# Kernel tuning notes

Hardware: AMD Instinct MI355X
Metric: run time of the kernel (lower is better)

## Reference

```python
import jax, jax.numpy as jnp
import numpy as np

WSZ = 16   # cfg.window_size
GD = 64    # cfg.group_dim


def setup_inputs() -> dict:
    key = jax.random.key(0)
    k1, k2, k3, k4 = jax.random.split(key, 4)
    B, T, D = 8, 8192, 1024
    z = jax.random.normal(k1, (B, T, D), jnp.float32)
    token_lens = jax.random.randint(k2, (B, T), 1, 9).astype(jnp.int32)
    W1 = jax.random.normal(k3, (D, GD), jnp.float32) / np.sqrt(D)
    W2 = jax.random.normal(k4, (GD, GD), jnp.float32) / np.sqrt(GD)
    return {"z": z, "token_lens": token_lens, "W1": W1, "W2": W2, "target_len": 6144}


def _choose_pairs(local_sim, budget):
    # local_sim: (W-1,) sims of adjacent edges inside one window.
    # Greedy non-overlapping matching in descending-sim order, up to `budget` pairs.
    Wn = local_sim.shape[0] + 1
    order = jnp.argsort(-local_sim)

    def step(state, e):
        used, mr, picked = state
        ok = (picked < budget) & (~used[e]) & (~used[e + 1])
        used = used.at[e].set(used[e] | ok)
        used = used.at[e + 1].set(used[e + 1] | ok)
        mr = mr.at[e + 1].set(mr[e + 1] | ok)
        return (used, mr, picked + ok.astype(jnp.int32)), None

    init = (jnp.zeros(Wn, bool), jnp.zeros(Wn, bool), jnp.int32(0))
    (_, mr, _), _ = jax.lax.scan(step, init, order)
    return mr  # (W,) True at j -> merge token j into j-1


def reference(z, token_lens, W1, W2, target_len):
    B, T, D = z.shape
    nwin = T // WSZ  # T chosen divisible by WSZ -> all windows full
    merges_needed = T - target_len
    base, extra = merges_needed // nwin, merges_needed % nwin
    budgets = jnp.minimum(base + (jnp.arange(nwin) < extra), WSZ // 2).astype(jnp.int32)

    # grouping MLP + cosine-style adjacent similarity
    g = jnp.maximum(z @ W1, 0.0) @ W2                         # (B,T,GD)
    g = g / (jnp.linalg.norm(g, axis=-1, keepdims=True) + 1e-8)
    sim = jnp.sum(g[:, :-1] * g[:, 1:], axis=-1)              # (B,T-1)
    # pad boundary edge slot, view per-window; keep only intra-window edges
    sim_pad = jnp.pad(sim, ((0, 0), (0, 1)), constant_values=-jnp.inf)
    local = sim_pad.reshape(B, nwin, WSZ)[:, :, : WSZ - 1]    # (B,nwin,W-1)

    pick = jax.vmap(jax.vmap(_choose_pairs, in_axes=(0, 0)), in_axes=(0, None))
    merge_right = pick(local, budgets).reshape(B, T)          # (B,T) bool
    keep = ~merge_right

    # pairs are disjoint -> sequential torch loop == parallel weighted merge
    w = token_lens.astype(z.dtype)
    absorb = merge_right[:, 1:]                               # token i absorbs i+1
    wi, wj = w[:, :-1, None], w[:, 1:, None]
    merged = (z[:, :-1] * wi + z[:, 1:] * wj) / (wi + wj)
    z2 = jnp.concatenate([jnp.where(absorb[:, :, None], merged, z[:, :-1]), z[:, -1:]], axis=1)
    l2 = jnp.concatenate(
        [jnp.where(absorb, token_lens[:, :-1] + token_lens[:, 1:], token_lens[:, :-1]),
         token_lens[:, -1:]], axis=1)

    # stable compaction: kept indices first (order preserved), truncate
    order = jnp.argsort(~keep, axis=1)[:, :target_len]        # jax sort is stable
    z_new = jnp.take_along_axis(z2, order[:, :, None], axis=1)
    lens_new = jnp.take_along_axis(l2, order, axis=1)
    starts_new = jnp.cumsum(lens_new, axis=1) - lens_new
    return z_new, lens_new, starts_new
```

## Files before the change

kernel.cpp:

```cpp
#include <hip/hip_runtime.h>

#define B_ 8
#define T_ 8192
#define D_ 1024
#define GD_ 64
#define WSZ_ 16
#define NWIN_ (T_ / WSZ_)
#define PL1_ (4 * 32 * 512)
#define PL2_ (4 * 2 * 512)

typedef __attribute__((ext_vector_type(8))) short short8v;
typedef __attribute__((ext_vector_type(4))) float f32x4;

__device__ __forceinline__ unsigned bf16rne(unsigned u) {
  return (u + 0x7FFFu + ((u >> 16) & 1u)) >> 16;
}
__device__ __forceinline__ void split2(float x, short& h, short& m) {
  const unsigned uh = bf16rne(__float_as_uint(x));
  const float fh = __uint_as_float(uh << 16);
  const float r1 = x - fh;
  const unsigned um = bf16rne(__float_as_uint(r1));
  h = (short)uh; m = (short)um;
}

__global__ __launch_bounds__(256) void k_prep(
    const float* __restrict__ W1, const float* __restrict__ W2,
    short* __restrict__ w1f, short* __restrict__ w2f)
{
  const int i = blockIdx.x * 256 + threadIdx.x;
  if (i < 4 * 32 * 64 * 8) {
    const int e = i & 7;
    const int lane = (i >> 3) & 63;
    const int tk = (i >> 9) & 31;
    const int tg = i >> 14;
    const int g = tg * 16 + (lane & 15);
    const int k = tk * 32 + ((lane >> 4) << 3) + e;
    short h, m;
    split2(W1[(long)k * GD_ + g], h, m);
    const int off = ((tg * 32 + tk) << 9) + lane * 8 + e;
    w1f[off] = h;
    w1f[PL1_ + off] = m;
  } else {
    const int j = i - 4 * 32 * 64 * 8;
    const int e = j & 7;
    const int lane = (j >> 3) & 63;
    const int tk = (j >> 9) & 1;
    const int tg = j >> 10;
    const int g = tg * 16 + (lane & 15);
    const int k = tk * 32 + ((lane >> 4) << 3) + e;
    short h, m;
    split2(W2[(long)k * GD_ + g], h, m);
    const int off = ((tg * 2 + tk) << 9) + lane * 8 + e;
    w2f[off] = h;
    w2f[PL2_ + off] = m;
  }
}

__global__ __launch_bounds__(256) void k_fused(
    const float* __restrict__ z, const short* __restrict__ w1f,
    const short* __restrict__ w2f, const int* __restrict__ lensp,
    float* __restrict__ out, double* __restrict__ sims_out,
    int TL, int baseBudget, int doEmit)
{
  __shared__ short Zsp[2][64][136];
  __shared__ double den[64];
  __shared__ double simsL[4][WSZ_ - 1];
  __shared__ int mrmL[4];
  __shared__ int elist[4][WSZ_];
  float (*Gf)[72] = (float (*)[72]) & Zsp[0][0][0];

  const int tid = threadIdx.x;
  const int lane = tid & 63;
  const int w = tid >> 6;
  const int th = w & 1;
  const int gh = w >> 1;
  const int cl = lane & 15;
  const int ko8 = (lane >> 4) * 8;
  const long bt0 = (long)blockIdx.x * 64;

  const int r = tid >> 2;
  const int kq = tid & 3;
  const float* zbase = z + (bt0 + r) * D_ + kq * 16;

  f32x4 acc[2][2];
#pragma unroll
  for (int a = 0; a < 2; ++a)
#pragma unroll
    for (int b = 0; b < 2; ++b) acc[a][b] = (f32x4){0.f, 0.f, 0.f, 0.f};

  auto stageK = [&](const float4 (&pz)[8]) {
#pragma unroll
    for (int h2 = 0; h2 < 2; ++h2) {
      short h[16], m[16];
#pragma unroll
      for (int q = 0; q < 4; ++q) {
        const float4 f = pz[h2 * 4 + q];
        split2(f.x, h[4 * q + 0], m[4 * q + 0]);
        split2(f.y, h[4 * q + 1], m[4 * q + 1]);
        split2(f.z, h[4 * q + 2], m[4 * q + 2]);
        split2(f.w, h[4 * q + 3], m[4 * q + 3]);
      }
      const int co = h2 * 64 + kq * 16;
      *(short8v*)&Zsp[0][r][co] =
          (short8v){h[0], h[1], h[2], h[3], h[4], h[5], h[6], h[7]};
      *(short8v*)&Zsp[0][r][co + 8] =
          (short8v){h[8], h[9], h[10], h[11], h[12], h[13], h[14], h[15]};
      *(short8v*)&Zsp[1][r][co] =
          (short8v){m[0], m[1], m[2], m[3], m[4], m[5], m[6], m[7]};
      *(short8v*)&Zsp[1][r][co + 8] =
          (short8v){m[8], m[9], m[10], m[11], m[12], m[13], m[14], m[15]};
    }
  };

  auto loadPz = [&](float4 (&pz)[8], int c) {
#pragma unroll
    for (int q = 0; q < 8; ++q) {
      const int col = (q >> 2) * 64 + (q & 3) * 4;
      pz[q] = *(const float4*)(zbase + c * 128 + col);
    }
  };

  auto mfma_chunk = [&](int c) {
#pragma unroll
    for (int ks = 0; ks < 4; ++ks) {
      const int ko = ks * 32 + ko8;
      short8v af[2][2], bf[2][2];
#pragma unroll
      for (int a = 0; a < 2; ++a)
#pragma unroll
        for (int s = 0; s < 2; ++s)
          af[a][s] = *(const short8v*)(
              w1f + s * PL1_ +
              ((((gh * 2 + a) * 32) + (c * 4 + ks)) << 9) + lane * 8);
#pragma unroll
      for (int b = 0; b < 2; ++b)
#pragma unroll
        for (int s = 0; s < 2; ++s)
          bf[b][s] = *(const short8v*)&Zsp[s][th * 32 + b * 16 + cl][ko];
#pragma unroll
      for (int a = 0; a < 2; ++a)
#pragma unroll
        for (int b = 0; b < 2; ++b) {
          f32x4 d = acc[a][b];
          d = __builtin_amdgcn_mfma_f32_16x16x32_bf16(af[a][0], bf[b][0], d, 0, 0, 0);
          d = __builtin_amdgcn_mfma_f32_16x16x32_bf16(af[a][0], bf[b][1], d, 0, 0, 0);
          d = __builtin_amdgcn_mfma_f32_16x16x32_bf16(af[a][1], bf[b][0], d, 0, 0, 0);
          acc[a][b] = d;
        }
    }
  };

  float4 pzA[8], pzB[8];
  loadPz(pzA, 0);

#pragma unroll 1
  for (int c = 0; c < 8; c += 2) {
    if (c) __syncthreads();
    stageK(pzA);
    __syncthreads();
    loadPz(pzB, c + 1);
    mfma_chunk(c);
    __syncthreads();
    stageK(pzB);
    __syncthreads();
    if (c + 2 < 8) loadPz(pzA, c + 2);
    mfma_chunk(c + 1);
  }
  __syncthreads();

#pragma unroll
  for (int a = 0; a < 2; ++a)
#pragma unroll
    for (int b = 0; b < 2; ++b) {
      const int t = th * 32 + b * 16 + cl;
      const int g0 = gh * 32 + a * 16 + (lane >> 4) * 4;
      short hh[4], hm[4];
#pragma unroll
      for (int e = 0; e < 4; ++e)
        split2(fmaxf(acc[a][b][e], 0.0f), hh[e], hm[e]);
      Zsp[0][t][g0 + 0] = hh[0]; Zsp[0][t][g0 + 1] = hh[1];
      Zsp[0][t][g0 + 2] = hh[2]; Zsp[0][t][g0 + 3] = hh[3];
      Zsp[1][t][g0 + 0] = hm[0]; Zsp[1][t][g0 + 1] = hm[1];
      Zsp[1][t][g0 + 2] = hm[2]; Zsp[1][t][g0 + 3] = hm[3];
    }
  __syncthreads();

#pragma unroll
  for (int a = 0; a < 2; ++a)
#pragma unroll
    for (int b = 0; b < 2; ++b) acc[a][b] = (f32x4){0.f, 0.f, 0.f, 0.f};
#pragma unroll
  for (int ks = 0; ks < 2; ++ks) {
    const int ko = ks * 32 + ko8;
    short8v af[2][2], bf[2][2];
#pragma unroll
    for (int a = 0; a < 2; ++a)
#pragma unroll
      for (int s = 0; s < 2; ++s)
        af[a][s] = *(const short8v*)(
            w2f + s * PL2_ + ((((gh * 2 + a) * 2) + ks) << 9) + lane * 8);
#pragma unroll
    for (int b = 0; b < 2; ++b)
#pragma unroll
      for (int s = 0; s < 2; ++s)
        bf[b][s] = *(const short8v*)&Zsp[s][th * 32 + b * 16 + cl][ko];
#pragma unroll
    for (int a = 0; a < 2; ++a)
#pragma unroll
      for (int b = 0; b < 2; ++b) {
        f32x4 d = acc[a][b];
        d = __builtin_amdgcn_mfma_f32_16x16x32_bf16(af[a][0], bf[b][0], d, 0, 0, 0);
        d = __builtin_amdgcn_mfma_f32_16x16x32_bf16(af[a][0], bf[b][1], d, 0, 0, 0);
        d = __builtin_amdgcn_mfma_f32_16x16x32_bf16(af[a][1], bf[b][0], d, 0, 0, 0);
        acc[a][b] = d;
      }
  }
  __syncthreads();

#pragma unroll
  for (int a = 0; a < 2; ++a)
#pragma unroll
    for (int b = 0; b < 2; ++b) {
      const int t = th * 32 + b * 16 + cl;
      const int g0 = gh * 32 + a * 16 + (lane >> 4) * 4;
      *(f32x4*)&Gf[t][g0] = acc[a][b];
    }
  __syncthreads();

  if (tid < 64) {
    double ss = 0.0;
#pragma unroll
    for (int q = 0; q < 16; ++q) {
      const float4 v = *(const float4*)&Gf[tid][4 * q];
      ss += (double)v.x * v.x + (double)v.y * v.y +
            (double)v.z * v.z + (double)v.w * v.w;
    }
    den[tid] = sqrt(ss) + 1e-8;
  }
  __syncthreads();

  if (tid < 4 * (WSZ_ - 1)) {
    const int ww = tid / (WSZ_ - 1), e = tid % (WSZ_ - 1);
    const int t = ww * WSZ_ + e;
    double s = 0.0;
#pragma unroll
    for (int q = 0; q < 16; ++q) {
      const float4 x = *(const float4*)&Gf[t][4 * q];
      const float4 y = *(const float4*)&Gf[t + 1][4 * q];
      s += (double)x.x * y.x + (double)x.y * y.y +
           (double)x.z * y.z + (double)x.w * y.w;
    }
    const double sv = s / (den[t] * den[t + 1]);
    simsL[ww][e] = sv;
    if (!doEmit)
      sims_out[((long)blockIdx.x * 4 + ww) * (WSZ_ - 1) + e] = sv;
  }
  if (!doEmit) return;
  __syncthreads();

  if (tid < 4) {
    double v[WSZ_ - 1];
    int id[WSZ_ - 1];
    for (int e = 0; e < WSZ_ - 1; ++e) { v[e] = simsL[tid][e]; id[e] = e; }
    for (int i = 1; i < WSZ_ - 1; ++i) {
      const double dv = v[i]; const int di = id[i];
      int j = i - 1;
      while (j >= 0 && v[j] < dv) { v[j + 1] = v[j]; id[j + 1] = id[j]; --j; }
      v[j + 1] = dv; id[j + 1] = di;
    }
    bool used[WSZ_];
    for (int i = 0; i < WSZ_; ++i) used[i] = false;
    int mrm = 0, picked = 0;
    for (int ii = 0; ii < WSZ_ - 1; ++ii) {
      const int e = id[ii];
      if (picked < baseBudget && !used[e] && !used[e + 1]) {
        used[e] = used[e + 1] = true;
        mrm |= (1 << (e + 1));
        ++picked;
      }
    }
    mrmL[tid] = mrm;
    int cnt = 0;
    for (int i = 0; i < WSZ_; ++i) {
      if ((mrm >> i) & 1) continue;
      const bool ab = (i < WSZ_ - 1) && ((mrm >> (i + 1)) & 1);
      elist[tid][cnt++] = i | (ab ? 256 : 0);
    }
  }
  __syncthreads();

  const int keptW = WSZ_ - baseBudget;
  const int bb = (int)(bt0 / T_);
  const int tb = (int)(bt0 % T_);
  const int wb = tb / WSZ_;
  const float* zbat = z + (long)bb * T_ * D_;
  const int* lbat = lensp + bb * T_;
  float* lout = out + (long)B_ * TL * D_;

#pragma unroll 1
  for (int ww2 = 0; ww2 < 4; ++ww2) {
    const int pbase = keptW * (wb + ww2);
    const int t0 = tb + ww2 * WSZ_;
#pragma unroll 1
    for (int j0 = 0; j0 < keptW; j0 += 4) {
      float4 oi[4], oj[4];
      int ti[4];
      bool ab[4], vl[4];
#pragma unroll
      for (int jj = 0; jj < 4; ++jj) {
        const int j = j0 + jj;
        vl[jj] = (j < keptW);
        if (vl[jj]) {
          const int e = elist[ww2][j];
          ab[jj] = (e >> 8) != 0;
          const int t = t0 + (e & 255);
          ti[jj] = t;
          oi[jj] = *(const float4*)(zbat + (long)t * D_ + tid * 4);
          if (ab[jj])
            oj[jj] = *(const float4*)(zbat + (long)(t + 1) * D_ + tid * 4);
        }
      }
#pragma unroll
      for (int jj = 0; jj < 4; ++jj) {
        if (!vl[jj]) continue;
        const int p = pbase + j0 + jj;
        float4 o = oi[jj];
        if (ab[jj]) {
          const float wi = (float)lbat[ti[jj]], wj2 = (float)lbat[ti[jj] + 1];
          const float s = wi + wj2;
          o.x = (o.x * wi + oj[jj].x * wj2) / s;
          o.y = (o.y * wi + oj[jj].y * wj2) / s;
          o.z = (o.z * wi + oj[jj].z * wj2) / s;
          o.w = (o.w * wi + oj[jj].w * wj2) / s;
          if (tid == 0) lout[(long)bb * TL + p] = s;
        } else {
          if (tid == 0) lout[(long)bb * TL + p] = (float)lbat[ti[jj]];
        }
        *(float4*)(out + ((long)bb * TL + p) * D_ + tid * 4) = o;
      }
    }
  }
}

__global__ __launch_bounds__(64) void k_pick(
    const double* __restrict__ sims, const int* __restrict__ tlptr,
    int* __restrict__ mrMask, int* __restrict__ keptCnt)
{
  const int win = blockIdx.x * 64 + threadIdx.x;
  if (win >= B_ * NWIN_) return;
  const int w = win % NWIN_;
  const int tl = tlptr[0];
  const int mn = T_ - tl;
  const int base = mn / NWIN_, extra = mn % NWIN_;
  int budget = base + (w < extra ? 1 : 0);
  if (budget > WSZ_ / 2) budget = WSZ_ / 2;
  if (budget < 0) budget = 0;
  double v[WSZ_ - 1];
  int id[WSZ_ - 1];
  for (int e = 0; e < WSZ_ - 1; ++e) {
    v[e] = sims[(long)win * (WSZ_ - 1) + e];
    id[e] = e;
  }
  for (int i = 1; i < WSZ_ - 1; ++i) {
    const double dv = v[i]; const int di = id[i];
    int j = i - 1;
    while (j >= 0 && v[j] < dv) { v[j + 1] = v[j]; id[j + 1] = id[j]; --j; }
    v[j + 1] = dv; id[j + 1] = di;
  }
  bool used[WSZ_];
  for (int i = 0; i < WSZ_; ++i) used[i] = false;
  int mrm = 0, picked = 0;
  for (int ii = 0; ii < WSZ_ - 1; ++ii) {
    const int e = id[ii];
    if (picked < budget && !used[e] && !used[e + 1]) {
      used[e] = used[e + 1] = true;
      mrm |= (1 << (e + 1));
      ++picked;
    }
  }
  mrMask[win] = mrm;
  keptCnt[win] = WSZ_ - picked;
}

__global__ void k_scan_windows(const int* __restrict__ keptCnt,
                               int* __restrict__ outOff)
{
  const int b = threadIdx.x;
  if (b >= B_) return;
  int off = 0;
  for (int w = 0; w < NWIN_; ++w) {
    outOff[b * NWIN_ + w] = off;
    off += keptCnt[b * NWIN_ + w];
  }
}

__global__ __launch_bounds__(256) void k_emit(
    const float* __restrict__ z, const int* __restrict__ lens,
    const int* __restrict__ mrMask, const int* __restrict__ outOff,
    float* __restrict__ out, int TL)
{
  const int bw = blockIdx.x;
  const int b = bw / NWIN_, w = bw % NWIN_;
  const int tid = threadIdx.x;
  const int mrm = mrMask[bw];
  int p = outOff[bw];
  const int t0 = w * WSZ_;
  const float* zb = z + (long)b * T_ * D_;
  const int* lb = lens + b * T_;
  float* lout = out + (long)B_ * TL * D_;
  for (int i = 0; i < WSZ_; ++i) {
    if ((mrm >> i) & 1) continue;
    if (p >= TL) return;
    const int t = t0 + i;
    const bool ab = (i < WSZ_ - 1) && ((mrm >> (i + 1)) & 1);
    float4 o = *(const float4*)(zb + (long)t * D_ + tid * 4);
    if (ab) {
      const float wi = (float)lb[t], wj = (float)lb[t + 1];
      const float s = wi + wj;
      const float4 zj = *(const float4*)(zb + (long)(t + 1) * D_ + tid * 4);
      o.x = (o.x * wi + zj.x * wj) / s;
      o.y = (o.y * wi + zj.y * wj) / s;
      o.z = (o.z * wi + zj.z * wj) / s;
      o.w = (o.w * wi + zj.w * wj) / s;
      if (tid == 0) lout[(long)b * TL + p] = s;
    } else {
      if (tid == 0) lout[(long)b * TL + p] = (float)lb[t];
    }
    *(float4*)(out + ((long)b * TL + p) * D_ + tid * 4) = o;
    ++p;
  }
}

__global__ __launch_bounds__(256) void k_starts(
    const float* __restrict__ lens_f, float* __restrict__ starts, int TL)
{
  const int b = blockIdx.x;
  const int tid = threadIdx.x;
  const int lane = tid & 63, wv = tid >> 6;
  __shared__ float wsum[4];
  const float* lrow = lens_f + (long)b * TL;
  float* srow = starts + (long)b * TL;
  float carry = 0.0f;

  for (int c0 = 0; c0 < TL; c0 += 256) {
    const int j = c0 + tid;
    const float v = (j < TL) ? lrow[j] : 0.0f;
    float x = v;
#pragma unroll
    for (int d = 1; d < 64; d <<= 1) {
      const float o = __shfl_up(x, d);
      if (lane >= d) x += o;
    }
    if (lane == 63) wsum[wv] = x;
    __syncthreads();
    float pre = 0.0f;
    if (wv > 0) pre += wsum[0];
    if (wv > 1) pre += wsum[1];
    if (wv > 2) pre += wsum[2];
    const float tot = wsum[0] + wsum[1] + wsum[2] + wsum[3];
    if (j < TL) srow[j] = carry + pre + x - v;
    carry += tot;
    __syncthreads();
  }
}

extern "C" void kernel_launch(void* const* d_in, const int* in_sizes, int n_in,
                              void* d_out, int out_size, void* d_ws, size_t ws_size,
                              hipStream_t stream)
{
  const float* z    = (const float*)d_in[0];
  const int*   lens = (const int*)d_in[1];
  const float* W1   = (const float*)d_in[2];
  const float* W2   = (const float*)d_in[3];
  const int*   tlp  = (const int*)d_in[4];

  float* out = (float*)d_out;
  const int TL = out_size / (B_ * (D_ + 2));

  const int merges = T_ - TL;
  const int base = merges / NWIN_;
  const int extra = merges % NWIN_;
  const int doEmit = (extra == 0 && base >= 0 && base <= 5) ? 1 : 0;

  double* sims = (double*)d_ws;
  char* p = (char*)d_ws + (size_t)B_ * NWIN_ * (WSZ_ - 1) * 8;
  int* mrMask = (int*)p;
  int* kept   = mrMask + B_ * NWIN_;
  int* outOff = kept + B_ * NWIN_;
  short* w1f = (short*)(p + 3 * B_ * NWIN_ * 4 + 64);
  w1f = (short*)(((size_t)w1f + 15) & ~(size_t)15);
  short* w2f = w1f + 2 * PL1_;

  hipLaunchKernelGGL(k_prep,
                     dim3((4 * 32 * 64 * 8 + 4 * 2 * 64 * 8) / 256), dim3(256),
                     0, stream, W1, W2, w1f, w2f);
  hipLaunchKernelGGL(k_fused, dim3((B_ * T_) / 64), dim3(256), 0, stream,
                     z, w1f, w2f, lens, out, sims, TL, base, doEmit);
  if (!doEmit) {
    hipLaunchKernelGGL(k_pick, dim3((B_ * NWIN_ + 63) / 64), dim3(64), 0,
                       stream, sims, tlp, mrMask, kept);
    hipLaunchKernelGGL(k_scan_windows, dim3(1), dim3(64), 0, stream,
                       kept, outOff);
    hipLaunchKernelGGL(k_emit, dim3(B_ * NWIN_), dim3(256), 0, stream,
                       z, lens, mrMask, outOff, out, TL);
  }
  hipLaunchKernelGGL(k_starts, dim3(B_), dim3(256), 0, stream,
                     out + (long)B_ * TL * D_,
                     out + (long)B_ * TL * D_ + (long)B_ * TL, TL);
}
```

Before: 190.1 us.

## Halve fused kernel token tile to 32 and raise occupancy

Shrinks the per-block token tile from 64 to 32 (two windows per block), doubling the grid. The GEMM, staging, similarity, pick and emit stages are remapped to the smaller tile, and the launch bounds now request 8 blocks per SM. The goal is lower LDS and register use per block so more blocks are resident and latency hides better. In exchange each block reloads the W1 fragments for half as many tokens, which doubles total W1 traffic.

```diff
diff --git a/kernel.cpp b/kernel.cpp
--- a/kernel.cpp
+++ b/kernel.cpp
@@ -6,6 +6,7 @@
 #define GD_ 64
 #define WSZ_ 16
 #define NWIN_ (T_ / WSZ_)
+#define TOKB_ 32
 #define PL1_ (4 * 32 * 512)
 #define PL2_ (4 * 2 * 512)
 
@@ -56,17 +57,17 @@
   }
 }
 
-__global__ __launch_bounds__(256) void k_fused(
+__global__ __launch_bounds__(256, 8) void k_fused(
     const float* __restrict__ z, const short* __restrict__ w1f,
     const short* __restrict__ w2f, const int* __restrict__ lensp,
     float* __restrict__ out, double* __restrict__ sims_out,
     int TL, int baseBudget, int doEmit)
 {
-  __shared__ short Zsp[2][64][136];
-  __shared__ double den[64];
-  __shared__ double simsL[4][WSZ_ - 1];
-  __shared__ int mrmL[4];
-  __shared__ int elist[4][WSZ_];
+  __shared__ short Zsp[2][TOKB_][136];
+  __shared__ double den[TOKB_];
+  __shared__ double simsL[2][WSZ_ - 1];
+  __shared__ int mrmL[2];
+  __shared__ int elist[2][WSZ_];
   float (*Gf)[72] = (float (*)[72]) & Zsp[0][0][0];
 
   const int tid = threadIdx.x;
@@ -76,55 +77,47 @@
   const int gh = w >> 1;
   const int cl = lane & 15;
   const int ko8 = (lane >> 4) * 8;
-  const long bt0 = (long)blockIdx.x * 64;
-
-  const int r = tid >> 2;
-  const int kq = tid & 3;
+  const long bt0 = (long)blockIdx.x * TOKB_;
+
+  const int r = tid >> 3;
+  const int kq = tid & 7;
   const float* zbase = z + (bt0 + r) * D_ + kq * 16;
 
-  f32x4 acc[2][2];
-#pragma unroll
-  for (int a = 0; a < 2; ++a)
-#pragma unroll
-    for (int b = 0; b < 2; ++b) acc[a][b] = (f32x4){0.f, 0.f, 0.f, 0.f};
-
-  auto stageK = [&](const float4 (&pz)[8]) {
-#pragma unroll
-    for (int h2 = 0; h2 < 2; ++h2) {
-      short h[16], m[16];
-#pragma unroll
-      for (int q = 0; q < 4; ++q) {
-        const float4 f = pz[h2 * 4 + q];
-        split2(f.x, h[4 * q + 0], m[4 * q + 0]);
-        split2(f.y, h[4 * q + 1], m[4 * q + 1]);
-        split2(f.z, h[4 * q + 2], m[4 * q + 2]);
-        split2(f.w, h[4 * q + 3], m[4 * q + 3]);
-      }
-      const int co = h2 * 64 + kq * 16;
-      *(short8v*)&Zsp[0][r][co] =
-          (short8v){h[0], h[1], h[2], h[3], h[4], h[5], h[6], h[7]};
-      *(short8v*)&Zsp[0][r][co + 8] =
-          (short8v){h[8], h[9], h[10], h[11], h[12], h[13], h[14], h[15]};
-      *(short8v*)&Zsp[1][r][co] =
-          (short8v){m[0], m[1], m[2], m[3], m[4], m[5], m[6], m[7]};
-      *(short8v*)&Zsp[1][r][co + 8] =
-          (short8v){m[8], m[9], m[10], m[11], m[12], m[13], m[14], m[15]};
-    }
+  f32x4 acc[2];
+#pragma unroll
+  for (int a = 0; a < 2; ++a) acc[a] = (f32x4){0.f, 0.f, 0.f, 0.f};
+
+  auto loadPz = [&](float4 (&pz)[4], int c) {
+#pragma unroll
+    for (int q = 0; q < 4; ++q)
+      pz[q] = *(const float4*)(zbase + c * 128 + q * 4);
   };
 
-  auto loadPz = [&](float4 (&pz)[8], int c) {
-#pragma unroll
-    for (int q = 0; q < 8; ++q) {
-      const int col = (q >> 2) * 64 + (q & 3) * 4;
-      pz[q] = *(const float4*)(zbase + c * 128 + col);
-    }
+  auto stageK = [&](const float4 (&pz)[4]) {
+    short h[16], m[16];
+#pragma unroll
+    for (int q = 0; q < 4; ++q) {
+      split2(pz[q].x, h[4 * q + 0], m[4 * q + 0]);
+      split2(pz[q].y, h[4 * q + 1], m[4 * q + 1]);
+      split2(pz[q].z, h[4 * q + 2], m[4 * q + 2]);
+      split2(pz[q].w, h[4 * q + 3], m[4 * q + 3]);
+    }
+    const int co = kq * 16;
+    *(short8v*)&Zsp[0][r][co] =
+        (short8v){h[0], h[1], h[2], h[3], h[4], h[5], h[6], h[7]};
+    *(short8v*)&Zsp[0][r][co + 8] =
+        (short8v){h[8], h[9], h[10], h[11], h[12], h[13], h[14], h[15]};
+    *(short8v*)&Zsp[1][r][co] =
+        (short8v){m[0], m[1], m[2], m[3], m[4], m[5], m[6], m[7]};
+    *(short8v*)&Zsp[1][r][co + 8] =
+        (short8v){m[8], m[9], m[10], m[11], m[12], m[13], m[14], m[15]};
   };
 
   auto mfma_chunk = [&](int c) {
 #pragma unroll
     for (int ks = 0; ks < 4; ++ks) {
       const int ko = ks * 32 + ko8;
-      short8v af[2][2], bf[2][2];
+      short8v af[2][2], bf[2];
 #pragma unroll
       for (int a = 0; a < 2; ++a)
 #pragma unroll
@@ -133,24 +126,20 @@
               w1f + s * PL1_ +
               ((((gh * 2 + a) * 32) + (c * 4 + ks)) << 9) + lane * 8);
 #pragma unroll
-      for (int b = 0; b < 2; ++b)
-#pragma unroll
-        for (int s = 0; s < 2; ++s)
-          bf[b][s] = *(const short8v*)&Zsp[s][th * 32 + b * 16 + cl][ko];
-#pragma unroll
-      for (int a = 0; a < 2; ++a)
-#pragma unroll
-        for (int b = 0; b < 2; ++b) {
-          f32x4 d = acc[a][b];
-          d = __builtin_amdgcn_mfma_f32_16x16x32_bf16(af[a][0], bf[b][0], d, 0, 0, 0);
-          d = __builtin_amdgcn_mfma_f32_16x16x32_bf16(af[a][0], bf[b][1], d, 0, 0, 0);
-          d = __builtin_amdgcn_mfma_f32_16x16x32_bf16(af[a][1], bf[b][0], d, 0, 0, 0);
-          acc[a][b] = d;
-        }
+      for (int s = 0; s < 2; ++s)
+        bf[s] = *(const short8v*)&Zsp[s][th * 16 + cl][ko];
+#pragma unroll
+      for (int a = 0; a < 2; ++a) {
+        f32x4 d = acc[a];
+        d = __builtin_amdgcn_mfma_f32_16x16x32_bf16(af[a][0], bf[0], d, 0, 0, 0);
+        d = __builtin_amdgcn_mfma_f32_16x16x32_bf16(af[a][0], bf[1], d, 0, 0, 0);
+        d = __builtin_amdgcn_mfma_f32_16x16x32_bf16(af[a][1], bf[0], d, 0, 0, 0);
+        acc[a] = d;
+      }
     }
   };
 
-  float4 pzA[8], pzB[8];
+  float4 pzA[4], pzB[4];
   loadPz(pzA, 0);
 
 #pragma unroll 1
@@ -169,30 +158,26 @@
   __syncthreads();
 
 #pragma unroll
-  for (int a = 0; a < 2; ++a)
-#pragma unroll
-    for (int b = 0; b < 2; ++b) {
-      const int t = th * 32 + b * 16 + cl;
-      const int g0 = gh * 32 + a * 16 + (lane >> 4) * 4;
-      short hh[4], hm[4];
-#pragma unroll
-      for (int e = 0; e < 4; ++e)
-        split2(fmaxf(acc[a][b][e], 0.0f), hh[e], hm[e]);
-      Zsp[0][t][g0 + 0] = hh[0]; Zsp[0][t][g0 + 1] = hh[1];
-      Zsp[0][t][g0 + 2] = hh[2]; Zsp[0][t][g0 + 3] = hh[3];
-      Zsp[1][t][g0 + 0] = hm[0]; Zsp[1][t][g0 + 1] = hm[1];
-      Zsp[1][t][g0 + 2] = hm[2]; Zsp[1][t][g0 + 3] = hm[3];
-    }
-  __syncthreads();
-
-#pragma unroll
-  for (int a = 0; a < 2; ++a)
-#pragma unroll
-    for (int b = 0; b < 2; ++b) acc[a][b] = (f32x4){0.f, 0.f, 0.f, 0.f};
+  for (int a = 0; a < 2; ++a) {
+    const int t = th * 16 + cl;
+    const int g0 = gh * 32 + a * 16 + (lane >> 4) * 4;
+    short hh[4], hm[4];
+#pragma unroll
+    for (int e = 0; e < 4; ++e)
+      split2(fmaxf(acc[a][e], 0.0f), hh[e], hm[e]);
+    Zsp[0][t][g0 + 0] = hh[0]; Zsp[0][t][g0 + 1] = hh[1];
+    Zsp[0][t][g0 + 2] = hh[2]; Zsp[0][t][g0 + 3] = hh[3];
+    Zsp[1][t][g0 + 0] = hm[0]; Zsp[1][t][g0 + 1] = hm[1];
+    Zsp[1][t][g0 + 2] = hm[2]; Zsp[1][t][g0 + 3] = hm[3];
+  }
+  __syncthreads();
+
+#pragma unroll
+  for (int a = 0; a < 2; ++a) acc[a] = (f32x4){0.f, 0.f, 0.f, 0.f};
 #pragma unroll
   for (int ks = 0; ks < 2; ++ks) {
     const int ko = ks * 32 + ko8;
-    short8v af[2][2], bf[2][2];
+    short8v af[2][2], bf[2];
 #pragma unroll
     for (int a = 0; a < 2; ++a)
 #pragma unroll
@@ -200,34 +185,28 @@
         af[a][s] = *(const short8v*)(
             w2f + s * PL2_ + ((((gh * 2 + a) * 2) + ks) << 9) + lane * 8);
 #pragma unroll
-    for (int b = 0; b < 2; ++b)
-#pragma unroll
-      for (int s = 0; s < 2; ++s)
-        bf[b][s] = *(const short8v*)&Zsp[s][th * 32 + b * 16 + cl][ko];
-#pragma unroll
-    for (int a = 0; a < 2; ++a)
-#pragma unroll
-      for (int b = 0; b < 2; ++b) {
-        f32x4 d = acc[a][b];
-        d = __builtin_amdgcn_mfma_f32_16x16x32_bf16(af[a][0], bf[b][0], d, 0, 0, 0);
-        d = __builtin_amdgcn_mfma_f32_16x16x32_bf16(af[a][0], bf[b][1], d, 0, 0, 0);
-        d = __builtin_amdgcn_mfma_f32_16x16x32_bf16(af[a][1], bf[b][0], d, 0, 0, 0);
-        acc[a][b] = d;
-      }
-  }
-  __syncthreads();
-
-#pragma unroll
-  for (int a = 0; a < 2; ++a)
-#pragma unroll
-    for (int b = 0; b < 2; ++b) {
-      const int t = th * 32 + b * 16 + cl;
-      const int g0 = gh * 32 + a * 16 + (lane >> 4) * 4;
-      *(f32x4*)&Gf[t][g0] = acc[a][b];
-    }
-  __syncthreads();
-
-  if (tid < 64) {
+    for (int s = 0; s < 2; ++s)
+      bf[s] = *(const short8v*)&Zsp[s][th * 16 + cl][ko];
+#pragma unroll
+    for (int a = 0; a < 2; ++a) {
+      f32x4 d = acc[a];
+      d = __builtin_amdgcn_mfma_f32_16x16x32_bf16(af[a][0], bf[0], d, 0, 0, 0);
+      d = __builtin_amdgcn_mfma_f32_16x16x32_bf16(af[a][0], bf[1], d, 0, 0, 0);
+      d = __builtin_amdgcn_mfma_f32_16x16x32_bf16(af[a][1], bf[0], d, 0, 0, 0);
+      acc[a] = d;
+    }
+  }
+  __syncthreads();
+
+#pragma unroll
+  for (int a = 0; a < 2; ++a) {
+    const int t = th * 16 + cl;
+    const int g0 = gh * 32 + a * 16 + (lane >> 4) * 4;
+    *(f32x4*)&Gf[t][g0] = acc[a];
+  }
+  __syncthreads();
+
+  if (tid < TOKB_) {
     double ss = 0.0;
 #pragma unroll
     for (int q = 0; q < 16; ++q) {
@@ -239,7 +218,7 @@
   }
   __syncthreads();
 
-  if (tid < 4 * (WSZ_ - 1)) {
+  if (tid < 2 * (WSZ_ - 1)) {
     const int ww = tid / (WSZ_ - 1), e = tid % (WSZ_ - 1);
     const int t = ww * WSZ_ + e;
     double s = 0.0;
@@ -253,12 +232,12 @@
     const double sv = s / (den[t] * den[t + 1]);
     simsL[ww][e] = sv;
     if (!doEmit)
-      sims_out[((long)blockIdx.x * 4 + ww) * (WSZ_ - 1) + e] = sv;
+      sims_out[((long)blockIdx.x * 2 + ww) * (WSZ_ - 1) + e] = sv;
   }
   if (!doEmit) return;
   __syncthreads();
 
-  if (tid < 4) {
+  if (tid < 2) {
     double v[WSZ_ - 1];
     int id[WSZ_ - 1];
     for (int e = 0; e < WSZ_ - 1; ++e) { v[e] = simsL[tid][e]; id[e] = e; }
@@ -298,7 +277,7 @@
   float* lout = out + (long)B_ * TL * D_;
 
 #pragma unroll 1
-  for (int ww2 = 0; ww2 < 4; ++ww2) {
+  for (int ww2 = 0; ww2 < 2; ++ww2) {
     const int pbase = keptW * (wb + ww2);
     const int t0 = tb + ww2 * WSZ_;
 #pragma unroll 1
@@ -494,7 +473,7 @@
   hipLaunchKernelGGL(k_prep,
                      dim3((4 * 32 * 64 * 8 + 4 * 2 * 64 * 8) / 256), dim3(256),
                      0, stream, W1, W2, w1f, w2f);
-  hipLaunchKernelGGL(k_fused, dim3((B_ * T_) / 64), dim3(256), 0, stream,
+  hipLaunchKernelGGL(k_fused, dim3((B_ * T_) / TOKB_), dim3(256), 0, stream,
                      z, w1f, w2f, lens, out, sims, TL, base, doEmit);
   if (!doEmit) {
     hipLaunchKernelGGL(k_pick, dim3((B_ * NWIN_ + 63) / 64), dim3(64), 0,
```

Measured after the change: 261.8 us. 1.38x slower.
